# Performance work log

Measured on AMD Instinct MI355X. Metric: run time of the kernel, lower is better.

The kernel has to match this reference:

```python
import jax, jax.numpy as jnp
import numpy as np

N = 4194304          # total elements
NUM_IDS = 262144     # sorted ids drawn from [0, NUM_IDS)
M_CAP = NUM_IDS + 1  # static upper bound on number of runs (sorted input)
L_CAP = 128          # static upper bound on run length (safe for this distribution)


def setup_inputs() -> dict:
    key = jax.random.key(0)
    k1, k2 = jax.random.split(key)
    ids = jnp.sort(jax.random.randint(k1, (N,), 0, NUM_IDS, dtype=jnp.int32))
    features = jax.random.normal(k2, (N,), dtype=jnp.float32)
    return {"ids": ids, "features": features}


def _group(ids, features):
    """Run-length grouping of consecutive equal ids into a padded [M_CAP, L_CAP] layout.
    Faithful to the tf.scan original: the FINAL run is never emitted (it stays in state).
    Rows beyond the valid runs are zero-filled; their ids are -1 (the original's sentinel).
    """
    n = ids.shape[0]
    ar = jnp.arange(n, dtype=jnp.int32)
    # boundary detection -> run index per element via prefix sum
    is_start = jnp.concatenate([jnp.ones((1,), bool), ids[1:] != ids[:-1]])
    seg = jnp.cumsum(is_start.astype(jnp.int32)) - 1      # [N] run id per element
    num_runs = seg[-1] + 1
    valid_seg = seg < (num_runs - 1)                        # drop last run (scan never emits it)
    # start position of each run (segment-min of element index)
    starts = jnp.full((M_CAP,), n, dtype=jnp.int32).at[seg].min(ar)
    pos = ar - starts[seg]                                  # [N] position within run
    ok = valid_seg & (pos < L_CAP)
    seg_idx = jnp.where(ok, seg, M_CAP)                     # out-of-range -> dropped
    padded = jnp.zeros((M_CAP, L_CAP), features.dtype).at[seg_idx, pos].set(features, mode='drop')
    run_ids = jnp.full((M_CAP,), -1, dtype=ids.dtype).at[jnp.where(valid_seg, seg, M_CAP)].set(ids, mode='drop')
    return run_ids, padded


def reference(ids, features):
    return _group(ids, features)
```

## Files before the change

### kernel.cpp

```cpp
#include <hip/hip_runtime.h>

#define N_ELEM   4194304
#define NUM_IDS  262144
#define M_CAP    (NUM_IDS + 1)
#define L_CAP    128

#define NTILES   2048
#define TILE     2048
#define NTHR     256
#define EPT      8

#define WS_TICKET 0
#define WS_TILES  4

#define ST_SHIFT  30
#define ST_AGG    (1u << ST_SHIFT)
#define ST_PRE    (3u << ST_SHIFT)
#define VAL_MASK  ((1u << ST_SHIFT) - 1u)
#define POISON    0xAAAAAAAAu

#define P_TOTAL   (M_CAP * L_CAP)
#define OUT_TOTAL ((size_t)M_CAP + P_TOTAL)

__global__ void __launch_bounds__(NTHR, 8)
k_fused(const int* __restrict__ ids,
        const float* __restrict__ feat,
        float* __restrict__ out,
        unsigned int* __restrict__ ws) {
    __shared__ int lds_start[TILE + 1];
    __shared__ int smw[4];
    __shared__ int bc[2];

    const int t    = threadIdx.x;
    const int lane = t & 63;
    const int wid  = t >> 6;

    if (t == 0) bc[0] = (int)(atomicAdd(&ws[WS_TICKET], 1u) - POISON);
    __syncthreads();
    const int vt = bc[0];
    const int tile_base = vt * TILE;
    const int tile_end  = tile_base + TILE;
    const int base      = tile_base + t * EPT;

    int v[EPT];
    {
        const int4* p4 = (const int4*)(ids + base);
        int4 a = p4[0], b4 = p4[1];
        v[0]=a.x; v[1]=a.y; v[2]=a.z; v[3]=a.w;
        v[4]=b4.x; v[5]=b4.y; v[6]=b4.z; v[7]=b4.w;
    }
    const int prev = (base == 0) ? -1 : ids[base - 1];

    unsigned flagbits = 0;
    int c = 0;
#pragma unroll
    for (int j = 0; j < EPT; ++j) {
        int f = (v[j] != ((j == 0) ? prev : v[j - 1]));
        flagbits |= ((unsigned)f << j);
        c += f;
    }

    int inc = c;
#pragma unroll
    for (int off = 1; off < 64; off <<= 1) {
        int nb = __shfl_up(inc, off);
        if (lane >= off) inc += nb;
    }
    if (lane == 63) smw[wid] = inc;
    __syncthreads();
    int wbase = 0, tot = 0;
#pragma unroll
    for (int w = 0; w < 4; ++w) {
        int s = smw[w];
        tot += s;
        if (w < wid) wbase += s;
    }
    const int excl = wbase + inc - c;
    const int cnt  = tot;

    if (t == 0) {
        unsigned w = (vt == 0) ? (ST_PRE | (unsigned)cnt) : (ST_AGG | (unsigned)cnt);
        __hip_atomic_store(&ws[WS_TILES + vt], w, __ATOMIC_RELAXED,
                           __HIP_MEMORY_SCOPE_AGENT);
    }

    {
        int r = excl;
#pragma unroll
        for (int j = 0; j < EPT; ++j)
            if (flagbits & (1u << j)) lds_start[r++] = base + j;
    }
    __syncthreads();

    if (wid == 1 && cnt > 0) {
        int e = tile_end;
        if (vt != NTILES - 1) {
            int s_last = lds_start[cnt - 1];
            if (tile_end - s_last < L_CAP) {
                int vid = ids[s_last];
                int m0 = (ids[tile_end + lane]      != vid);
                int m1 = (ids[tile_end + lane + 64] != vid);
                unsigned long long b0 = __ballot(m0);
                unsigned long long b1 = __ballot(m1);
                int ext;
                if (b0)      ext = __ffsll(b0) - 1;
                else if (b1) ext = 64 + __ffsll(b1) - 1;
                else         ext = 128;
                e = tile_end + ext;
            }
        }
        if (lane == 0) lds_start[cnt] = e;
    }

    if (wid == 0) {
        int prefix = 0;
        if (vt > 0) {
            int look = vt - 1;
            for (;;) {
                int idx = look - lane;
                unsigned w = ST_PRE;
                if (idx >= 0)
                    w = __hip_atomic_load(&ws[WS_TILES + idx], __ATOMIC_RELAXED,
                                          __HIP_MEMORY_SCOPE_AGENT);
                unsigned st = w >> ST_SHIFT;
                unsigned long long preB = __ballot(st == 3u);
                unsigned long long invB = __ballot((st & 1u) == 0u);
                if (preB) {
                    int lp = __ffsll(preB) - 1;
                    if (!(invB & ((lp > 0) ? ((1ull << lp) - 1ull) : 0ull))) {
                        int contrib = (lane <= lp) ? (int)(w & VAL_MASK) : 0;
                        for (int o = 32; o; o >>= 1) contrib += __shfl_down(contrib, o);
                        prefix += __shfl(contrib, 0);
                        break;
                    }
                } else if (!invB) {
                    int contrib = (int)(w & VAL_MASK);
                    for (int o = 32; o; o >>= 1) contrib += __shfl_down(contrib, o);
                    prefix += __shfl(contrib, 0);
                    look -= 64;
                    continue;
                }
                __builtin_amdgcn_s_sleep(1);
            }
        }
        if (lane == 0) {
            bc[1] = prefix;
            __hip_atomic_store(&ws[WS_TILES + vt],
                               ST_PRE | (unsigned)(prefix + cnt),
                               __ATOMIC_RELAXED, __HIP_MEMORY_SCOPE_AGENT);
        }
    }
    __syncthreads();

    const int prefix = bc[1];
    const bool last  = (vt == NTILES - 1);
    int cnt_emit = last ? cnt - 1 : cnt;
    if (cnt_emit < 0) cnt_emit = 0;

    const size_t q_lo = (size_t)M_CAP + (size_t)prefix * L_CAP;
    if (cnt_emit > 0) {
        if (t < 3)  out[q_lo + t] = 0.0f;
        if (t == 3) out[q_lo + (size_t)cnt_emit * L_CAP - 1] = 0.0f;
        float* qa = out + q_lo + 3;
        const int nf4 = cnt_emit * 32 - 1;
        const float4 z = {0.0f, 0.0f, 0.0f, 0.0f};
        for (int u = t; u < nf4; u += NTHR)
            *(float4*)(qa + 4 * (size_t)u) = z;
    }
    __syncthreads();

    {
        float fv[EPT];
        const float4* f4 = (const float4*)(feat + base);
        float4 fa = f4[0], fb = f4[1];
        fv[0]=fa.x; fv[1]=fa.y; fv[2]=fa.z; fv[3]=fa.w;
        fv[4]=fb.x; fv[5]=fb.y; fv[6]=fb.z; fv[7]=fb.w;

        int r = excl - 1;
        int s_cur = (r >= 0) ? lds_start[r] : base - 100000;
#pragma unroll
        for (int j = 0; j < EPT; ++j) {
            if (flagbits & (1u << j)) {
                ++r; s_cur = base + j;
                if (!(last && r == cnt - 1))
                    out[prefix + r] = (float)v[j];
            }
            int pos = base + j - s_cur;
            if (pos < L_CAP && r >= 0 && !(last && r == cnt - 1))
                out[q_lo + (size_t)r * L_CAP + pos] = fv[j];
        }
    }

    if (wid == 2 && cnt > 0 && !last) {
        int s_last = lds_start[cnt - 1];
        int nExt   = lds_start[cnt] - tile_end;
        size_t rowb = q_lo + (size_t)(cnt - 1) * L_CAP;
#pragma unroll
        for (int p = 0; p < 2; ++p) {
            int k = lane + 64 * p;
            int pos = tile_end + k - s_last;
            if (k < nExt && pos < L_CAP)
                out[rowb + pos] = feat[tile_end + k];
        }
    }

    if (last) {
        const int num_valid = prefix + cnt_emit;
        for (int i = num_valid + t; i < M_CAP; i += NTHR)
            out[i] = -1.0f;
        const size_t p0 = (size_t)M_CAP + (size_t)num_valid * L_CAP;
        for (size_t p = p0 + t; p < OUT_TOTAL; p += NTHR)
            out[p] = 0.0f;
    }
}

extern "C" void kernel_launch(void* const* d_in, const int* in_sizes, int n_in,
                              void* d_out, int out_size, void* d_ws, size_t ws_size,
                              hipStream_t stream) {
    const int* ids    = (const int*)d_in[0];
    const float* feat = (const float*)d_in[1];
    float* out        = (float*)d_out;
    unsigned int* ws  = (unsigned int*)d_ws;

    k_fused<<<NTILES, NTHR, 0, stream>>>(ids, feat, out, ws);
}
```

Measured before the change: 199.6 us.

## Stage padded rows in LDS and write them out with coalesced float4 stores

The padded feature rows are now assembled in a shared-memory buffer in chunks of 64 runs and then written to global memory with aligned float4 stores. Before, the kernel zero-filled each row in global memory and then scattered feature writes on top of it. This removes the double write and the uncoalesced scatter to global memory. Run starts are stored as 16-bit offsets, and the launch-bounds occupancy hint drops from 8 to 4 because the LDS buffer is now about 32KB, which lowers the number of resident workgroups.

```diff
diff --git a/kernel.cpp b/kernel.cpp
--- a/kernel.cpp
+++ b/kernel.cpp
@@ -9,6 +9,7 @@
 #define TILE     2048
 #define NTHR     256
 #define EPT      8
+#define CH       64
 
 #define WS_TICKET 0
 #define WS_TILES  4
@@ -22,12 +23,13 @@
 #define P_TOTAL   (M_CAP * L_CAP)
 #define OUT_TOTAL ((size_t)M_CAP + P_TOTAL)
 
-__global__ void __launch_bounds__(NTHR, 8)
+__global__ void __launch_bounds__(NTHR, 4)
 k_fused(const int* __restrict__ ids,
         const float* __restrict__ feat,
         float* __restrict__ out,
         unsigned int* __restrict__ ws) {
-    __shared__ int lds_start[TILE + 1];
+    __shared__ __align__(16) float lds_buf[CH * L_CAP - 4];
+    __shared__ unsigned short lds_sta[TILE + 2];
     __shared__ int smw[4];
     __shared__ int bc[2];
 
@@ -43,11 +45,16 @@
     const int base      = tile_base + t * EPT;
 
     int v[EPT];
+    float fv[EPT];
     {
         const int4* p4 = (const int4*)(ids + base);
         int4 a = p4[0], b4 = p4[1];
         v[0]=a.x; v[1]=a.y; v[2]=a.z; v[3]=a.w;
         v[4]=b4.x; v[5]=b4.y; v[6]=b4.z; v[7]=b4.w;
+        const float4* f4 = (const float4*)(feat + base);
+        float4 fa = f4[0], fb = f4[1];
+        fv[0]=fa.x; fv[1]=fa.y; fv[2]=fa.z; fv[3]=fa.w;
+        fv[4]=fb.x; fv[5]=fb.y; fv[6]=fb.z; fv[7]=fb.w;
     }
     const int prev = (base == 0) ? -1 : ids[base - 1];
 
@@ -84,18 +91,26 @@
                            __HIP_MEMORY_SCOPE_AGENT);
     }
 
+    int rr[EPT], pp[EPT];
     {
-        int r = excl;
-#pragma unroll
-        for (int j = 0; j < EPT; ++j)
-            if (flagbits & (1u << j)) lds_start[r++] = base + j;
+        int r = excl - 1;
+        int s_cur = base - 100000;
+#pragma unroll
+        for (int j = 0; j < EPT; ++j) {
+            if (flagbits & (1u << j)) {
+                ++r; s_cur = base + j;
+                lds_sta[r] = (unsigned short)(s_cur - tile_base);
+            }
+            rr[j] = r;
+            pp[j] = base + j - s_cur;
+        }
     }
     __syncthreads();
 
     if (wid == 1 && cnt > 0) {
-        int e = tile_end;
+        int e_rel = TILE;
         if (vt != NTILES - 1) {
-            int s_last = lds_start[cnt - 1];
+            int s_last = tile_base + (int)lds_sta[cnt - 1];
             if (tile_end - s_last < L_CAP) {
                 int vid = ids[s_last];
                 int m0 = (ids[tile_end + lane]      != vid);
@@ -106,10 +121,10 @@
                 if (b0)      ext = __ffsll(b0) - 1;
                 else if (b1) ext = 64 + __ffsll(b1) - 1;
                 else         ext = 128;
-                e = tile_end + ext;
-            }
-        }
-        if (lane == 0) lds_start[cnt] = e;
+                e_rel = TILE + ext;
+            }
+        }
+        if (lane == 0) lds_sta[cnt] = (unsigned short)e_rel;
     }
 
     if (wid == 0) {
@@ -157,51 +172,61 @@
     int cnt_emit = last ? cnt - 1 : cnt;
     if (cnt_emit < 0) cnt_emit = 0;
 
+    for (int r = t; r < cnt_emit; r += NTHR)
+        out[prefix + r] = (float)ids[tile_base + (int)lds_sta[r]];
+
     const size_t q_lo = (size_t)M_CAP + (size_t)prefix * L_CAP;
-    if (cnt_emit > 0) {
-        if (t < 3)  out[q_lo + t] = 0.0f;
-        if (t == 3) out[q_lo + (size_t)cnt_emit * L_CAP - 1] = 0.0f;
-        float* qa = out + q_lo + 3;
-        const int nf4 = cnt_emit * 32 - 1;
-        const float4 z = {0.0f, 0.0f, 0.0f, 0.0f};
-        for (int u = t; u < nf4; u += NTHR)
-            *(float4*)(qa + 4 * (size_t)u) = z;
-    }
-    __syncthreads();
-
-    {
-        float fv[EPT];
-        const float4* f4 = (const float4*)(feat + base);
-        float4 fa = f4[0], fb = f4[1];
-        fv[0]=fa.x; fv[1]=fa.y; fv[2]=fa.z; fv[3]=fa.w;
-        fv[4]=fb.x; fv[5]=fb.y; fv[6]=fb.z; fv[7]=fb.w;
-
-        int r = excl - 1;
-        int s_cur = (r >= 0) ? lds_start[r] : base - 100000;
+    float4* buf4 = (float4*)lds_buf;
+
+    for (int c0r = 0; c0r < cnt_emit; c0r += CH) {
+        const int nr    = min(CH, cnt_emit - c0r);
+        const int nbuf4 = nr * 32 - 1;
+
+        {
+            const float4 z = {0.0f, 0.0f, 0.0f, 0.0f};
+            for (int k = t; k < nbuf4; k += NTHR) buf4[k] = z;
+        }
+        if (t < 3) {
+            int s0 = (int)lds_sta[c0r];
+            int L0 = (int)lds_sta[c0r + 1] - s0; if (L0 > L_CAP) L0 = L_CAP;
+            out[q_lo + (size_t)c0r * L_CAP + t] =
+                (t < L0) ? feat[tile_base + s0 + t] : 0.0f;
+        }
+        if (t == 3) {
+            int sL = (int)lds_sta[c0r + nr - 1];
+            int LL = (int)lds_sta[c0r + nr] - sL; if (LL > L_CAP) LL = L_CAP;
+            out[q_lo + (size_t)(c0r + nr) * L_CAP - 1] =
+                (LL == L_CAP) ? feat[tile_base + sL + 127] : 0.0f;
+        }
+        __syncthreads();
+
 #pragma unroll
         for (int j = 0; j < EPT; ++j) {
-            if (flagbits & (1u << j)) {
-                ++r; s_cur = base + j;
-                if (!(last && r == cnt - 1))
-                    out[prefix + r] = (float)v[j];
-            }
-            int pos = base + j - s_cur;
-            if (pos < L_CAP && r >= 0 && !(last && r == cnt - 1))
-                out[q_lo + (size_t)r * L_CAP + pos] = fv[j];
-        }
-    }
-
-    if (wid == 2 && cnt > 0 && !last) {
-        int s_last = lds_start[cnt - 1];
-        int nExt   = lds_start[cnt] - tile_end;
-        size_t rowb = q_lo + (size_t)(cnt - 1) * L_CAP;
-#pragma unroll
-        for (int p = 0; p < 2; ++p) {
-            int k = lane + 64 * p;
-            int pos = tile_end + k - s_last;
-            if (k < nExt && pos < L_CAP)
-                out[rowb + pos] = feat[tile_end + k];
-        }
+            int r = rr[j] - c0r;
+            if ((unsigned)r < (unsigned)nr && pp[j] < L_CAP) {
+                int idx = r * L_CAP + pp[j] - 3;
+                if (idx >= 0 && idx < nbuf4 * 4) lds_buf[idx] = fv[j];
+            }
+        }
+        if (!last && cnt > 0 && t < 128) {
+            int re = (cnt - 1) - c0r;
+            if (re >= 0 && re < nr) {
+                int nExt = (int)lds_sta[cnt] - TILE;
+                int sl   = (int)lds_sta[cnt - 1];
+                int pos  = TILE + t - sl;
+                if (t < nExt && pos < L_CAP) {
+                    int idx = re * L_CAP + pos - 3;
+                    if (idx >= 0 && idx < nbuf4 * 4)
+                        lds_buf[idx] = feat[tile_end + t];
+                }
+            }
+        }
+        __syncthreads();
+
+        float* qb = out + q_lo + (size_t)c0r * L_CAP + 3;
+        for (int k = t; k < nbuf4; k += NTHR)
+            *(float4*)(qb + 4 * (size_t)k) = buf4[k];
+        __syncthreads();
     }
 
     if (last) {
```

Result: faster. 185.8 us (-6.9%).
